# Kernel optimization log

Measured on AMD Instinct MI355X. Metric: run time of the kernel, lower is better.

The kernel has to match this reference:

```python
import jax, jax.numpy as jnp
import numpy as np

N, DEG = 20000, 16          # nodes, fixed neighbor-list length
H, C, D, IN = 4, 16, 128, 256  # cluster_heads, num_centroids, hidden_dim, input_dim
NEG_SLOPE = 0.2


def setup_inputs() -> dict:
    key = jax.random.key(0)
    ks = jax.random.split(key, 12)
    s_in = 1.0 / np.sqrt(IN)
    s_h = 1.0 / np.sqrt(D)
    inp = {
        "x_node": jax.random.normal(ks[0], (N, IN), dtype=jnp.float32),
        "adj": jax.random.randint(ks[1], (N, DEG), 0, N, dtype=jnp.int32),
        "epoch": 1,
        # linear layers (torch convention: W [out, in])
        "W1": jax.random.uniform(ks[2], (D, IN), jnp.float32, -s_in, s_in),
        "b1": jax.random.uniform(ks[3], (D,), jnp.float32, -s_in, s_in),
        "W2": jax.random.uniform(ks[4], (D, D), jnp.float32, -s_h, s_h),
        "b2": jax.random.uniform(ks[5], (D,), jnp.float32, -s_h, s_h),
        "W21": jax.random.uniform(ks[6], (D, D), jnp.float32, -s_h, s_h),
        "b21": jax.random.uniform(ks[7], (D,), jnp.float32, -s_h, s_h),
        # centroids: 2*rand-1, shape [H, C*D]
        "centroids": 2.0 * jax.random.uniform(ks[8], (H, C * D), dtype=jnp.float32) - 1.0,
        # headConv: xavier_uniform gain=1.414 on [H, 1]
        "headConv": jax.random.uniform(ks[9], (H, 1), jnp.float32,
                                       -1.414 * np.sqrt(6.0 / (H + 1)),
                                       1.414 * np.sqrt(6.0 / (H + 1))),
    }
    return inp


def _leaky(x):
    return jnp.where(x >= 0, x, NEG_SLOPE * x)


def _cluster_block(h, adj, centroids, headConv):
    # h: [N, D]; adj: [N, deg]; centroids: [H, C*D]; headConv: [H, 1]
    cent = centroids.reshape(H, C, D)
    # squared L2 distance dist[h,c,n] = ||x_n - cent_hc||^2 (norm expansion,
    # avoids the [H,C,N,D] broadcast the torch code materializes)
    hn2 = jnp.sum(h * h, axis=-1)                      # [N]
    cn2 = jnp.sum(cent * cent, axis=-1)                # [H, C]
    cross = jnp.einsum('hcd,nd->hcn', cent, h)         # [H, C, N]
    dist = cn2[..., None] + hn2[None, None, :] - 2.0 * cross
    # nu=1: q = (1 + dist)^-1
    q = 1.0 / (1.0 + dist)                             # [H, C, N]
    # gather neighbor scores per node and normalize over the edge dim
    qn = q[:, :, adj]                                  # [H, C, N, deg]
    qn = qn / jnp.sum(qn, axis=3, keepdims=True)
    # combine heads with headConv, then softmax over edges per centroid
    w = jnp.einsum('hcne,h->nce', qn, headConv[:, 0])  # [N, C, deg]
    w = jax.nn.softmax(w, axis=2)
    # weighted aggregation of neighbor features
    new_feat = jnp.einsum('nce,ned->ncd', w, h[adj])   # [N, C, D]
    return new_feat


def reference(x_node, adj, epoch, W1, b1, W2, b2, W21, b21, centroids, headConv):
    # eval mode: dropout is identity
    x = _leaky(x_node @ W1.T + b1)
    h_prime = _leaky(x @ W2.T + b2)                    # [N, D]
    new_feat = _cluster_block(h_prime, adj, centroids, headConv)
    new_feat = _leaky(new_feat @ W21.T + b21)          # [N, C, D]
    return (h_prime, new_feat)
```

## Files before the change

kernel.cpp:

```cpp
#include <hip/hip_runtime.h>
#include <cstdint>
#include <cstddef>

#define NEG_SLOPE 0.2f

typedef __attribute__((ext_vector_type(8))) short bf16x8;
typedef __attribute__((ext_vector_type(8))) unsigned short u16x8;
typedef __attribute__((ext_vector_type(4))) unsigned short u16x4;
typedef __attribute__((ext_vector_type(4))) float f32x4;

__device__ __forceinline__ float leaky_f(float x) { return x >= 0.f ? x : NEG_SLOPE * x; }

__device__ __forceinline__ unsigned short f2bf(float f) {
    union { float f; uint32_t u; } v; v.f = f;
    return (unsigned short)((v.u + 0x7fffu + ((v.u >> 16) & 1u)) >> 16);
}
__device__ __forceinline__ float bf2f(unsigned short u) {
    union { uint32_t u; float f; } v; v.u = ((uint32_t)u) << 16; return v.f;
}
__device__ __forceinline__ float bfhi(uint32_t w) {
    union { uint32_t u; float f; } v; v.u = w & 0xffff0000u; return v.f;
}
__device__ __forceinline__ float bflo(uint32_t w) {
    union { uint32_t u; float f; } v; v.u = w << 16; return v.f;
}
__device__ __forceinline__ u16x8 cvt8(float4 a, float4 b) {
    u16x8 o;
    o[0] = f2bf(a.x); o[1] = f2bf(a.y); o[2] = f2bf(a.z); o[3] = f2bf(a.w);
    o[4] = f2bf(b.x); o[5] = f2bf(b.y); o[6] = f2bf(b.z); o[7] = f2bf(b.w);
    return o;
}

__global__ __launch_bounds__(256)
void pack_kernel(const float* __restrict__ x_node, const float* __restrict__ W1,
                 const float* __restrict__ W2, const float* __restrict__ W21,
                 const float* __restrict__ cent,
                 unsigned short* __restrict__ xb, unsigned short* __restrict__ pw1,
                 unsigned short* __restrict__ pw2, unsigned short* __restrict__ pw3,
                 float* __restrict__ cn2g, int N)
{
    const int bid = blockIdx.x, tid = threadIdx.x;
    if (bid < 36) {
        const int sub = tid >> 6, lane = tid & 63, g = bid * 4 + sub;
        const int l15 = lane & 15, l4 = lane >> 4;
        const float* src; unsigned short* dst;
        if (g < 64) {
            int step = g >> 3, f = g & 7;
            src = W1 + (size_t)(f * 16 + l15) * 256 + step * 32 + l4 * 8;
            dst = pw1 + ((size_t)(step * 8 + f) * 64 + lane) * 8;
        } else if (g < 96) {
            int gg = g - 64, step = gg >> 3, f = gg & 7;
            src = W2 + (size_t)(f * 16 + l15) * 128 + step * 32 + l4 * 8;
            dst = pw2 + ((size_t)(step * 8 + f) * 64 + lane) * 8;
        } else {
            int gg = g - 96, step = gg / 12, f = gg % 12;
            int brow = f * 16 + l15;
            const float* base = (brow < 128) ? (W21 + (size_t)brow * 128)
                                             : (cent + (size_t)(brow - 128) * 128);
            src = base + step * 32 + l4 * 8;
            dst = pw3 + ((size_t)(step * 12 + f) * 64 + lane) * 8;
        }
        float4 a = *reinterpret_cast<const float4*>(src);
        float4 b = *reinterpret_cast<const float4*>(src + 4);
        *reinterpret_cast<u16x8*>(dst) = cvt8(a, b);
    } else if (bid == 36) {
        int r = tid >> 2, c0 = (tid & 3) * 32;
        const float* cr = cent + (size_t)r * 128 + c0;
        float s = 0.f;
#pragma unroll
        for (int q = 0; q < 8; q++) {
            float4 v = *reinterpret_cast<const float4*>(cr + q * 4);
            s += v.x * v.x + v.y * v.y + v.z * v.z + v.w * v.w;
        }
        s += __shfl_xor(s, 1); s += __shfl_xor(s, 2);
        if ((tid & 3) == 0) cn2g[r] = s;
    } else {
        size_t base = (size_t)(bid - 37) * 4096 + (size_t)tid * 16;
        float4 v0 = *reinterpret_cast<const float4*>(x_node + base);
        float4 v1 = *reinterpret_cast<const float4*>(x_node + base + 4);
        float4 v2 = *reinterpret_cast<const float4*>(x_node + base + 8);
        float4 v3 = *reinterpret_cast<const float4*>(x_node + base + 12);
        *reinterpret_cast<u16x8*>(xb + base)     = cvt8(v0, v1);
        *reinterpret_cast<u16x8*>(xb + base + 8) = cvt8(v2, v3);
    }
}

__global__ __launch_bounds__(256)
void fused_gemms(const unsigned short* __restrict__ xb,
                 const unsigned short* __restrict__ pw1, const unsigned short* __restrict__ pw2,
                 const unsigned short* __restrict__ pw3,
                 const float* __restrict__ b1, const float* __restrict__ b2,
                 const float* __restrict__ cn2g,
                 float* __restrict__ h_out, unsigned short* __restrict__ hWb,
                 unsigned short* __restrict__ qtb, int N)
{
    __shared__ __align__(16) short Xs[16 * 136];
    __shared__ __align__(16) float hf32[16 * 132];
    __shared__ __align__(16) unsigned short hWs[16 * 136];
    __shared__ __align__(16) unsigned short qts[16 * 72];
    __shared__ float hn2s[4][16];

    const int tid = threadIdx.x, wave = tid >> 6, lane = tid & 63;
    const int l15 = lane & 15, l4 = lane >> 4;
    const int rowBlk = blockIdx.x * 16;

    f32x4 a0{0.f,0.f,0.f,0.f}, a1{0.f,0.f,0.f,0.f}, a2{0.f,0.f,0.f,0.f};
    {
        const unsigned short* ap = xb + (size_t)(rowBlk + l15) * 256 + l4 * 8;
        const unsigned short* bp = pw1 + (size_t)(wave * 2) * 512 + lane * 8;
#pragma unroll
        for (int k = 0; k < 8; k++) {
            bf16x8 af = *reinterpret_cast<const bf16x8*>(ap + k * 32);
            bf16x8 bf0 = *reinterpret_cast<const bf16x8*>(bp + (size_t)k * 8 * 512);
            bf16x8 bf1 = *reinterpret_cast<const bf16x8*>(bp + (size_t)k * 8 * 512 + 512);
            a0 = __builtin_amdgcn_mfma_f32_16x16x32_bf16(af, bf0, a0, 0, 0, 0);
            a1 = __builtin_amdgcn_mfma_f32_16x16x32_bf16(af, bf1, a1, 0, 0, 0);
        }
        float bia = b1[wave * 32 + l15], bib = b1[wave * 32 + 16 + l15];
#pragma unroll
        for (int j = 0; j < 4; j++) {
            Xs[(l4 * 4 + j) * 136 + wave * 32 + l15]      = (short)f2bf(leaky_f(a0[j] + bia));
            Xs[(l4 * 4 + j) * 136 + wave * 32 + 16 + l15] = (short)f2bf(leaky_f(a1[j] + bib));
        }
    }
    __syncthreads();

    a0 = f32x4{0.f,0.f,0.f,0.f}; a1 = f32x4{0.f,0.f,0.f,0.f};
    const short* xp = &Xs[l15 * 136 + l4 * 8];
    {
        const unsigned short* bp = pw2 + (size_t)(wave * 2) * 512 + lane * 8;
#pragma unroll
        for (int k = 0; k < 4; k++) {
            bf16x8 af = *reinterpret_cast<const bf16x8*>(xp + k * 32);
            bf16x8 bf0 = *reinterpret_cast<const bf16x8*>(bp + (size_t)k * 8 * 512);
            bf16x8 bf1 = *reinterpret_cast<const bf16x8*>(bp + (size_t)k * 8 * 512 + 512);
            a0 = __builtin_amdgcn_mfma_f32_16x16x32_bf16(af, bf0, a0, 0, 0, 0);
            a1 = __builtin_amdgcn_mfma_f32_16x16x32_bf16(af, bf1, a1, 0, 0, 0);
        }
    }
    float hv0[4], hv1[4], pn[4];
    {
        float bia = b2[wave * 32 + l15], bib = b2[wave * 32 + 16 + l15];
#pragma unroll
        for (int j = 0; j < 4; j++) {
            hv0[j] = leaky_f(a0[j] + bia);
            hv1[j] = leaky_f(a1[j] + bib);
            float s = hv0[j] * hv0[j] + hv1[j] * hv1[j];
            s += __shfl_xor(s, 1); s += __shfl_xor(s, 2);
            s += __shfl_xor(s, 4); s += __shfl_xor(s, 8);
            pn[j] = s;
        }
    }
    __syncthreads();

#pragma unroll
    for (int j = 0; j < 4; j++) {
        int r = l4 * 4 + j;
        hf32[r * 132 + wave * 32 + l15]      = hv0[j];
        hf32[r * 132 + wave * 32 + 16 + l15] = hv1[j];
        Xs[r * 136 + wave * 32 + l15]      = (short)f2bf(hv0[j]);
        Xs[r * 136 + wave * 32 + 16 + l15] = (short)f2bf(hv1[j]);
        if (l15 == 0) hn2s[wave][r] = pn[j];
    }
    __syncthreads();

    {
        int r = tid >> 4, c0 = (tid & 15) * 8;
        f32x4 v0 = *reinterpret_cast<const f32x4*>(&hf32[r * 132 + c0]);
        f32x4 v1 = *reinterpret_cast<const f32x4*>(&hf32[r * 132 + c0 + 4]);
        float* dst = h_out + (size_t)(rowBlk + r) * 128 + c0;
        __builtin_nontemporal_store(v0, reinterpret_cast<f32x4*>(dst));
        __builtin_nontemporal_store(v1, reinterpret_cast<f32x4*>(dst + 4));
    }

    a0 = f32x4{0.f,0.f,0.f,0.f}; a1 = f32x4{0.f,0.f,0.f,0.f}; a2 = f32x4{0.f,0.f,0.f,0.f};
    {
        const unsigned short* bp = pw3 + (size_t)(wave * 3) * 512 + lane * 8;
#pragma unroll
        for (int k = 0; k < 4; k++) {
            bf16x8 af = *reinterpret_cast<const bf16x8*>(xp + k * 32);
            bf16x8 bf0 = *reinterpret_cast<const bf16x8*>(bp + (size_t)k * 12 * 512);
            bf16x8 bf1 = *reinterpret_cast<const bf16x8*>(bp + (size_t)k * 12 * 512 + 512);
            bf16x8 bf2 = *reinterpret_cast<const bf16x8*>(bp + (size_t)k * 12 * 512 + 1024);
            a0 = __builtin_amdgcn_mfma_f32_16x16x32_bf16(af, bf0, a0, 0, 0, 0);
            a1 = __builtin_amdgcn_mfma_f32_16x16x32_bf16(af, bf1, a1, 0, 0, 0);
            a2 = __builtin_amdgcn_mfma_f32_16x16x32_bf16(af, bf2, a2, 0, 0, 0);
        }
    }
    {
        float hn2r[4];
#pragma unroll
        for (int j = 0; j < 4; j++)
            hn2r[j] = hn2s[0][l4 * 4 + j] + hn2s[1][l4 * 4 + j]
                    + hn2s[2][l4 * 4 + j] + hn2s[3][l4 * 4 + j];
        f32x4 av[3] = {a0, a1, a2};
#pragma unroll
        for (int ff = 0; ff < 3; ff++) {
            int col = wave * 48 + ff * 16 + l15;
            if (col < 128) {
#pragma unroll
                for (int j = 0; j < 4; j++)
                    hWs[(l4 * 4 + j) * 136 + col] = f2bf(av[ff][j]);
            } else {
                int c2 = col - 128;
                float cn2v = cn2g[c2];
#pragma unroll
                for (int j = 0; j < 4; j++) {
                    float q = 1.f / (1.f + cn2v + hn2r[j] - 2.f * av[ff][j]);
                    qts[(l4 * 4 + j) * 72 + c2] = f2bf(q);
                }
            }
        }
    }
    __syncthreads();

    {
        int r = tid >> 4, c0 = (tid & 15) * 8;
        *reinterpret_cast<u16x8*>(hWb + (size_t)(rowBlk + r) * 128 + c0) =
            *reinterpret_cast<const u16x8*>(&hWs[r * 136 + c0]);
        int cq = (tid & 15) * 4;
        *reinterpret_cast<u16x4*>(qtb + (size_t)(rowBlk + r) * 64 + cq) =
            *reinterpret_cast<const u16x4*>(&qts[r * 72 + cq]);
    }
}

__global__ __launch_bounds__(256)
void agg_kernel(const int* __restrict__ adj, const unsigned short* __restrict__ qtb,
                const unsigned short* __restrict__ hWb, const float* __restrict__ b21,
                const float* __restrict__ headConv, float* __restrict__ out1)
{
    __shared__ __align__(16) unsigned short qs[4][16 * 64];
    __shared__ __align__(16) unsigned short hs[4][16 * 128];
    __shared__ float wbuf[4][16][16];

    const int wv = threadIdx.x >> 6, lane = threadIdx.x & 63;
    const int n = blockIdx.x * 4 + wv;

    int myadj = adj[n * 16 + (lane & 15)];

#pragma unroll
    for (int i = 0; i < 2; i++) {
        int row = i * 8 + (lane >> 3);
        int nb = __shfl(myadj, row);
        *reinterpret_cast<u16x8*>(&qs[wv][i * 512 + lane * 8]) =
            *reinterpret_cast<const u16x8*>(qtb + (size_t)nb * 64 + (lane & 7) * 8);
    }
#pragma unroll
    for (int i = 0; i < 4; i++) {
        int row = i * 4 + (lane >> 4);
        int nb = __shfl(myadj, row);
        *reinterpret_cast<u16x8*>(&hs[wv][i * 512 + lane * 8]) =
            *reinterpret_cast<const u16x8*>(hWb + (size_t)nb * 128 + (lane & 15) * 8);
    }
    __syncthreads();

    {
        float qv[16];
        float s = 0.f;
#pragma unroll
        for (int e = 0; e < 16; e++) { qv[e] = bf2f(qs[wv][e * 64 + lane]); s += qv[e]; }
        float rs = 1.f / s;
        float conv = headConv[lane >> 4];
        float wn[16], m = -1e30f;
#pragma unroll
        for (int e = 0; e < 16; e++) {
            float t = conv * qv[e] * rs;
            t += __shfl_xor(t, 16);
            t += __shfl_xor(t, 32);
            wn[e] = t;
            m = fmaxf(m, t);
        }
        float sum = 0.f;
#pragma unroll
        for (int e = 0; e < 16; e++) { wn[e] = __expf(wn[e] - m); sum += wn[e]; }
        float inv = 1.f / sum;
        const int c = lane & 15, eg = lane >> 4;
#pragma unroll
        for (int j = 0; j < 4; j++) wbuf[wv][eg * 4 + j][c] = wn[eg * 4 + j] * inv;
    }
    __syncthreads();

    {
        const int dg = lane & 15, cg = lane >> 4, d0 = dg * 4;
        float bv[8];
        *reinterpret_cast<float4*>(bv)     = *reinterpret_cast<const float4*>(b21 + d0);
        *reinterpret_cast<float4*>(bv + 4) = *reinterpret_cast<const float4*>(b21 + d0 + 64);
        float acc[4][8];
#pragma unroll
        for (int jc = 0; jc < 4; jc++)
#pragma unroll
            for (int j = 0; j < 8; j++) acc[jc][j] = bv[j];

#pragma unroll
        for (int e = 0; e < 16; e++) {
            uint2 wlo = *reinterpret_cast<const uint2*>(&hs[wv][e * 128 + d0]);
            uint2 whi = *reinterpret_cast<const uint2*>(&hs[wv][e * 128 + 64 + d0]);
            float hv[8];
            hv[0] = bflo(wlo.x); hv[1] = bfhi(wlo.x); hv[2] = bflo(wlo.y); hv[3] = bfhi(wlo.y);
            hv[4] = bflo(whi.x); hv[5] = bfhi(whi.x); hv[6] = bflo(whi.y); hv[7] = bfhi(whi.y);
#pragma unroll
            for (int jc = 0; jc < 4; jc++) {
                float w = wbuf[wv][e][cg * 4 + jc];
#pragma unroll
                for (int j = 0; j < 8; j++) acc[jc][j] = fmaf(w, hv[j], acc[jc][j]);
            }
        }
#pragma unroll
        for (int jc = 0; jc < 4; jc++) {
            f32x4 lo, hi;
#pragma unroll
            for (int j = 0; j < 4; j++) { lo[j] = leaky_f(acc[jc][j]); hi[j] = leaky_f(acc[jc][j + 4]); }
            float* dst = out1 + ((size_t)(n * 16 + cg * 4 + jc)) * 128;
            __builtin_nontemporal_store(lo, reinterpret_cast<f32x4*>(dst + d0));
            __builtin_nontemporal_store(hi, reinterpret_cast<f32x4*>(dst + d0 + 64));
        }
    }
}

extern "C" void kernel_launch(void* const* d_in, const int* in_sizes, int n_in,
                              void* d_out, int out_size, void* d_ws, size_t ws_size,
                              hipStream_t stream)
{
    const float* x_node   = (const float*)d_in[0];
    const int*   adj      = (const int*)  d_in[1];
    const float* W1       = (const float*)d_in[3];
    const float* b1       = (const float*)d_in[4];
    const float* W2       = (const float*)d_in[5];
    const float* b2       = (const float*)d_in[6];
    const float* W21      = (const float*)d_in[7];
    const float* b21      = (const float*)d_in[8];
    const float* cent     = (const float*)d_in[9];
    const float* headConv = (const float*)d_in[10];

    const int N = in_sizes[0] / 256;

    float* h    = (float*)d_out;
    float* out1 = h + (size_t)N * 128;

    unsigned short* xb  = (unsigned short*)d_ws;
    unsigned short* hWb = xb  + (size_t)N * 256;
    unsigned short* qtb = hWb + (size_t)N * 128;
    unsigned short* pw1 = qtb + (size_t)N * 64;
    unsigned short* pw2 = pw1 + 32768;
    unsigned short* pw3 = pw2 + 16384;
    float*          cn2g = (float*)(pw3 + 24576);

    const int xblocks = (N * 256) / 4096;

    pack_kernel<<<37 + xblocks, 256, 0, stream>>>(x_node, W1, W2, W21, cent,
                                                  xb, pw1, pw2, pw3, cn2g, N);
    fused_gemms<<<N / 16, 256, 0, stream>>>(xb, pw1, pw2, pw3, b1, b2, cn2g,
                                            h, hWb, qtb, N);
    agg_kernel<<<N / 4, 256, 0, stream>>>(adj, qtb, hWb, b21, headConv, out1);
}
```

Baseline: 68.58 us.

## Drop block barriers in aggregation, use packed FMA and per-lane softmax

The aggregation kernel now keeps its per-wave LDS staging wave-local and drops both block-wide __syncthreads calls. It overlays the q tile and the softmax weights in one union to cut LDS footprint. The softmax max and sum become cross-lane shuffle reductions, so each lane computes only 4 exps instead of 16. The weighted sum uses packed two-wide FMA with a vectorized weight load. Correctness now relies on in-order LDS access within a wave, with no explicit barrier. The kernel is likely bounded by the large fp32 output store, which caps what these compute savings can give.

```diff
diff --git a/kernel.cpp b/kernel.cpp
--- a/kernel.cpp
+++ b/kernel.cpp
@@ -8,6 +8,7 @@
 typedef __attribute__((ext_vector_type(8))) unsigned short u16x8;
 typedef __attribute__((ext_vector_type(4))) unsigned short u16x4;
 typedef __attribute__((ext_vector_type(4))) float f32x4;
+typedef __attribute__((ext_vector_type(2))) float f32x2;
 
 __device__ __forceinline__ float leaky_f(float x) { return x >= 0.f ? x : NEG_SLOPE * x; }
 
@@ -30,6 +31,16 @@
     o[4] = f2bf(b.x); o[5] = f2bf(b.y); o[6] = f2bf(b.z); o[7] = f2bf(b.w);
     return o;
 }
+
+#if __has_builtin(__builtin_elementwise_fma)
+__device__ __forceinline__ f32x2 fma2(f32x2 a, f32x2 b, f32x2 c) {
+    return __builtin_elementwise_fma(a, b, c);
+}
+#else
+__device__ __forceinline__ f32x2 fma2(f32x2 a, f32x2 b, f32x2 c) {
+    f32x2 r; r[0] = fmaf(a[0], b[0], c[0]); r[1] = fmaf(a[1], b[1], c[1]); return r;
+}
+#endif
 
 __global__ __launch_bounds__(256)
 void pack_kernel(const float* __restrict__ x_node, const float* __restrict__ W1,
@@ -224,93 +235,114 @@
     }
 }
 
+struct PerWaveU {
+    union {
+        unsigned short qs[1024];
+        float wbuf[16][16];
+    };
+};
+
 __global__ __launch_bounds__(256)
 void agg_kernel(const int* __restrict__ adj, const unsigned short* __restrict__ qtb,
                 const unsigned short* __restrict__ hWb, const float* __restrict__ b21,
                 const float* __restrict__ headConv, float* __restrict__ out1)
 {
-    __shared__ __align__(16) unsigned short qs[4][16 * 64];
     __shared__ __align__(16) unsigned short hs[4][16 * 128];
-    __shared__ float wbuf[4][16][16];
+    __shared__ __align__(16) PerWaveU upw[4];
 
     const int wv = threadIdx.x >> 6, lane = threadIdx.x & 63;
+    const int eg = lane >> 4, l15 = lane & 15;
     const int n = blockIdx.x * 4 + wv;
 
-    int myadj = adj[n * 16 + (lane & 15)];
+    const int myadj = adj[n * 16 + l15];
 
 #pragma unroll
     for (int i = 0; i < 2; i++) {
         int row = i * 8 + (lane >> 3);
         int nb = __shfl(myadj, row);
-        *reinterpret_cast<u16x8*>(&qs[wv][i * 512 + lane * 8]) =
+        *reinterpret_cast<u16x8*>(&upw[wv].qs[i * 512 + lane * 8]) =
             *reinterpret_cast<const u16x8*>(qtb + (size_t)nb * 64 + (lane & 7) * 8);
     }
 #pragma unroll
     for (int i = 0; i < 4; i++) {
-        int row = i * 4 + (lane >> 4);
+        int row = i * 4 + eg;
         int nb = __shfl(myadj, row);
         *reinterpret_cast<u16x8*>(&hs[wv][i * 512 + lane * 8]) =
-            *reinterpret_cast<const u16x8*>(hWb + (size_t)nb * 128 + (lane & 15) * 8);
-    }
-    __syncthreads();
+            *reinterpret_cast<const u16x8*>(hWb + (size_t)nb * 128 + l15 * 8);
+    }
 
     {
         float qv[16];
         float s = 0.f;
 #pragma unroll
-        for (int e = 0; e < 16; e++) { qv[e] = bf2f(qs[wv][e * 64 + lane]); s += qv[e]; }
+        for (int e = 0; e < 16; e++) { qv[e] = bf2f(upw[wv].qs[e * 64 + lane]); s += qv[e]; }
         float rs = 1.f / s;
-        float conv = headConv[lane >> 4];
-        float wn[16], m = -1e30f;
+        float conv = headConv[eg];
+        float t[16];
 #pragma unroll
         for (int e = 0; e < 16; e++) {
-            float t = conv * qv[e] * rs;
-            t += __shfl_xor(t, 16);
-            t += __shfl_xor(t, 32);
-            wn[e] = t;
-            m = fmaxf(m, t);
-        }
-        float sum = 0.f;
-#pragma unroll
-        for (int e = 0; e < 16; e++) { wn[e] = __expf(wn[e] - m); sum += wn[e]; }
-        float inv = 1.f / sum;
-        const int c = lane & 15, eg = lane >> 4;
-#pragma unroll
-        for (int j = 0; j < 4; j++) wbuf[wv][eg * 4 + j][c] = wn[eg * 4 + j] * inv;
-    }
-    __syncthreads();
-
-    {
-        const int dg = lane & 15, cg = lane >> 4, d0 = dg * 4;
-        float bv[8];
-        *reinterpret_cast<float4*>(bv)     = *reinterpret_cast<const float4*>(b21 + d0);
-        *reinterpret_cast<float4*>(bv + 4) = *reinterpret_cast<const float4*>(b21 + d0 + 64);
-        float acc[4][8];
-#pragma unroll
-        for (int jc = 0; jc < 4; jc++)
-#pragma unroll
-            for (int j = 0; j < 8; j++) acc[jc][j] = bv[j];
+            float v = conv * qv[e] * rs;
+            v += __shfl_xor(v, 16);
+            v += __shfl_xor(v, 32);
+            t[e] = v;
+        }
+        float m = fmaxf(fmaxf(t[eg * 4], t[eg * 4 + 1]), fmaxf(t[eg * 4 + 2], t[eg * 4 + 3]));
+        m = fmaxf(m, __shfl_xor(m, 16));
+        m = fmaxf(m, __shfl_xor(m, 32));
+        float ex[4];
+        float ps = 0.f;
+#pragma unroll
+        for (int j = 0; j < 4; j++) { ex[j] = __expf(t[eg * 4 + j] - m); ps += ex[j]; }
+        ps += __shfl_xor(ps, 16);
+        ps += __shfl_xor(ps, 32);
+        float inv = 1.f / ps;
+#pragma unroll
+        for (int j = 0; j < 4; j++) upw[wv].wbuf[eg * 4 + j][l15] = ex[j] * inv;
+    }
+
+    {
+        const int d0 = l15 * 4;
+        float bvf[8];
+        *reinterpret_cast<float4*>(bvf)     = *reinterpret_cast<const float4*>(b21 + d0);
+        *reinterpret_cast<float4*>(bvf + 4) = *reinterpret_cast<const float4*>(b21 + d0 + 64);
+        f32x2 acc2[4][4];
+#pragma unroll
+        for (int jc = 0; jc < 4; jc++) {
+            acc2[jc][0] = f32x2{bvf[0], bvf[1]};
+            acc2[jc][1] = f32x2{bvf[2], bvf[3]};
+            acc2[jc][2] = f32x2{bvf[4], bvf[5]};
+            acc2[jc][3] = f32x2{bvf[6], bvf[7]};
+        }
 
 #pragma unroll
         for (int e = 0; e < 16; e++) {
             uint2 wlo = *reinterpret_cast<const uint2*>(&hs[wv][e * 128 + d0]);
             uint2 whi = *reinterpret_cast<const uint2*>(&hs[wv][e * 128 + 64 + d0]);
-            float hv[8];
-            hv[0] = bflo(wlo.x); hv[1] = bfhi(wlo.x); hv[2] = bflo(wlo.y); hv[3] = bfhi(wlo.y);
-            hv[4] = bflo(whi.x); hv[5] = bfhi(whi.x); hv[6] = bflo(whi.y); hv[7] = bfhi(whi.y);
+            float w4[4];
+            *reinterpret_cast<float4*>(w4) =
+                *reinterpret_cast<const float4*>(&upw[wv].wbuf[e][eg * 4]);
+            f32x2 hv2[4];
+            hv2[0] = f32x2{bflo(wlo.x), bfhi(wlo.x)};
+            hv2[1] = f32x2{bflo(wlo.y), bfhi(wlo.y)};
+            hv2[2] = f32x2{bflo(whi.x), bfhi(whi.x)};
+            hv2[3] = f32x2{bflo(whi.y), bfhi(whi.y)};
 #pragma unroll
             for (int jc = 0; jc < 4; jc++) {
-                float w = wbuf[wv][e][cg * 4 + jc];
-#pragma unroll
-                for (int j = 0; j < 8; j++) acc[jc][j] = fmaf(w, hv[j], acc[jc][j]);
+                f32x2 w2 = f32x2{w4[jc], w4[jc]};
+#pragma unroll
+                for (int q = 0; q < 4; q++)
+                    acc2[jc][q] = fma2(w2, hv2[q], acc2[jc][q]);
             }
         }
+
 #pragma unroll
         for (int jc = 0; jc < 4; jc++) {
             f32x4 lo, hi;
-#pragma unroll
-            for (int j = 0; j < 4; j++) { lo[j] = leaky_f(acc[jc][j]); hi[j] = leaky_f(acc[jc][j + 4]); }
-            float* dst = out1 + ((size_t)(n * 16 + cg * 4 + jc)) * 128;
+            lo[0] = leaky_f(acc2[jc][0][0]); lo[1] = leaky_f(acc2[jc][0][1]);
+            lo[2] = leaky_f(acc2[jc][1][0]); lo[3] = leaky_f(acc2[jc][1][1]);
+            hi[0] = leaky_f(acc2[jc][2][0]); hi[1] = leaky_f(acc2[jc][2][1]);
+            hi[2] = leaky_f(acc2[jc][3][0]); hi[3] = leaky_f(acc2[jc][3][1]);
+            float* dst = out1 + ((size_t)(n * 16 + eg * 4 + jc)) * 128;
             __builtin_nontemporal_store(lo, reinterpret_cast<f32x4*>(dst + d0));
             __builtin_nontemporal_store(hi, reinterpret_cast<f32x4*>(dst + d0 + 64));
         }
```

After: 65.24 us. -4.9%, faster.
